# Kernel tuning notes

Hardware: AMD Instinct MI355X
Metric: run time of the kernel (lower is better)

## Reference

```python
import jax, jax.numpy as jnp
import numpy as np


def pixel_coordinates(h, w):
    # (h, w, 2) grid of (x, y) in [-1, 1]
    y = jnp.linspace(-1.0, 1.0, h)
    x = jnp.linspace(-1.0, 1.0, w)
    yy, xx = jnp.meshgrid(y, x, indexing='ij')
    return jnp.stack([xx, yy], axis=-1)


def base_grid(h_in, w_in):
    y = jnp.linspace(-1.0 + 1.0 / h_in, 1.0 - 1.0 / h_in, h_in)
    x = jnp.linspace(-1.0 + 1.0 / w_in, 1.0 - 1.0 / w_in, w_in)
    yy, xx = jnp.meshgrid(y, x, indexing='ij')
    return jnp.stack([xx, yy], axis=-1)  # [h_in, w_in, 2]


def setup_inputs() -> dict:
    key = jax.random.key(0)
    params = jax.random.normal(key, (2, 9, 32, 32), dtype=jnp.float32)
    return {"params": params, "h_out": 128, "w_out": 128}


def reference(params, h_out, w_out):
    B, _, h_in, w_in = params.shape
    N = h_in * w_in
    p = jnp.transpose(params, (0, 2, 3, 1))  # [B, h_in, w_in, 9]

    # positions (mu): base grid + tanh(offset) * (2/h_in)
    mu = base_grid(h_in, w_in)[None] + jnp.tanh(p[..., 0:2]) * (2.0 / h_in)
    mu = mu.reshape(B, N, 2)

    # covariance via Cholesky-like factor L = [[exp(a), 0], [b, exp(c)]]
    v1x = jnp.exp(p[..., 2])
    v2x = p[..., 3]
    v2y = jnp.exp(p[..., 4])
    zero = jnp.zeros_like(v1x)
    L = jnp.stack([jnp.stack([v1x, zero], axis=-1),
                   jnp.stack([v2x, v2y], axis=-1)], axis=-2)  # [B,h,w,2,2]
    cov = L @ jnp.swapaxes(L, -1, -2)
    cov = cov.reshape(B, N, 2, 2) + jnp.eye(2, dtype=params.dtype) * 1e-5
    Sigma_inv = jnp.linalg.inv(cov)  # [B, N, 2, 2]

    colors = jax.nn.sigmoid(p[..., 5:8]).reshape(B, N, 3)
    opacities = jax.nn.sigmoid(p[..., 8]).reshape(B, N)

    coords = pixel_coordinates(h_out, w_out)  # [H, W, 2]
    dx = coords[None, None] - mu[:, :, None, None, :]  # [B, N, H, W, 2]
    exponent = -0.5 * jnp.einsum('bnhwi,bnij,bnhwj->bnhw', dx, Sigma_inv, dx)
    exponent = jnp.clip(exponent, -20.0, 20.0)
    kernel = jnp.exp(exponent)  # [B, N, H, W]

    weights = opacities[:, :, None, None] * kernel
    weights_sum = jnp.sum(weights, axis=1, keepdims=True) + 1e-8
    norm_w = weights / weights_sum  # [B, N, H, W]
    image = jnp.einsum('bnhw,bnc->bchw', norm_w, colors)  # [B, 3, H, W]
    return image
```

## Files before the change

### kernel.cpp

```cpp
#include <hip/hip_runtime.h>


#define NB   2
#define NG   1024
#define HOUT 128
#define WOUT 128
#define PSTRIDE 24
#define NCHUNK 16

typedef float v2f __attribute__((ext_vector_type(2)));

__device__ __forceinline__ float fast_exp(float x) {
    return __builtin_amdgcn_exp2f(x * 1.4426950408889634f);
}
__device__ __forceinline__ float fast_sigmoid(float x) {
    float e = __builtin_amdgcn_exp2f(-x * 1.4426950408889634f);
    return __builtin_amdgcn_rcpf(1.0f + e);
}
__device__ __forceinline__ float fast_tanh(float x) {
    float e = __builtin_amdgcn_exp2f(-x * 2.8853900817779268f);
    return fmaf(2.0f, __builtin_amdgcn_rcpf(1.0f + e), -1.0f);
}

__global__ __launch_bounds__(256) void gauss_setup(const float* __restrict__ params,
                                                   float* __restrict__ gd) {
    int gid = blockIdx.x * blockDim.x + threadIdx.x;
    if (gid >= NB * NG) return;
    int b = gid >> 10;
    int n = gid & (NG - 1);
    int h = n >> 5;
    int w = n & 31;

    const float* P = params + b * 9 * NG + n;
    float p0 = P[0 * NG];
    float p1 = P[1 * NG];
    float p2 = P[2 * NG];
    float p3 = P[3 * NG];
    float p4 = P[4 * NG];
    float p5 = P[5 * NG];
    float p6 = P[6 * NG];
    float p7 = P[7 * NG];
    float p8 = P[8 * NG];

    float mux = -0.96875f + (float)w * 0.0625f + fast_tanh(p0) * 0.0625f;
    float muy = -0.96875f + (float)h * 0.0625f + fast_tanh(p1) * 0.0625f;

    float ea  = fast_exp(p2);
    float ec  = fast_exp(p4);
    float c00 = ea * ea + 1e-5f;
    float c01 = p3 * ea;
    float c11 = p3 * p3 + ec * ec + 1e-5f;
    float det = c00 * c11 - c01 * c01;
    float id  = 1.0f / det;
    float Sa  =  c11 * id;
    float Sb  = -c01 * id;
    float Sc  =  c00 * id;

    const float s = -0.72134752044448169f;
    float A  = s * Sa;
    float B2 = 2.0f * s * Sb;
    float C  = s * Sc;

    float cr = fast_sigmoid(p5);
    float cg = fast_sigmoid(p6);
    float cb = fast_sigmoid(p7);
    float op = fast_sigmoid(p8);

    float* o = gd + ((size_t)b * (NG / 2) + (n >> 1)) * PSTRIDE + (n & 1);
    o[0]  = mux;  o[2]  = muy;  o[4]  = A;       o[6]  = B2;
    o[8]  = C;    o[10] = op;   o[12] = op * cr; o[14] = op * cg;
    o[16] = op * cb;
}

__global__ __launch_bounds__(1024, 8) void gauss_render(const float* __restrict__ gd,
                                                        float* __restrict__ out) {
    __shared__ float4 sred[1024];

    const int tx  = threadIdx.x;
    const int ty  = threadIdx.y;
    const int tid = ty * 64 + tx;
    const int blk = blockIdx.x;
    const int b   = blk >> 8;
    const int pix = ((blk & 255) << 6) + tx;

    const int h = pix >> 7;
    const int w = pix & 127;
    const float px = -1.0f + (float)w * (2.0f / 127.0f);
    const float py = -1.0f + (float)h * (2.0f / 127.0f);
    const v2f px2 = {px, px};
    const v2f py2 = {py, py};

    const int chunk = __builtin_amdgcn_readfirstlane(ty);
    const v2f* __restrict__ gp = (const v2f*)(gd
        + (size_t)b * (NG / 2) * PSTRIDE
        + (size_t)chunk * (NG / 2 / NCHUNK) * PSTRIDE);

    v2f wsum2 = {0.0f, 0.0f}, ar2 = {0.0f, 0.0f};
    v2f ag2   = {0.0f, 0.0f}, ab2 = {0.0f, 0.0f};

    #pragma unroll 4
    for (int j = 0; j < NG / 2 / NCHUNK; ++j) {
        const v2f* __restrict__ r = gp + j * (PSTRIDE / 2);
        v2f mux2 = r[0], muy2 = r[1];
        v2f A2   = r[2], B22  = r[3], C2 = r[4];
        v2f op2  = r[5], ocr2 = r[6], ocg2 = r[7], ocb2 = r[8];

        v2f dx = px2 - mux2;
        v2f dy = py2 - muy2;
        v2f m  = A2 * dx;
        m      = __builtin_elementwise_fma(B22, dy, m);
        v2f t  = C2 * dy;
        v2f e2 = __builtin_elementwise_fma(t, dy, m * dx);
        e2 = __builtin_elementwise_max(e2, (v2f){-28.853900817779268f,
                                                 -28.853900817779268f});
        v2f k2 = {__builtin_amdgcn_exp2f(e2.x), __builtin_amdgcn_exp2f(e2.y)};

        wsum2 = __builtin_elementwise_fma(op2,  k2, wsum2);
        ar2   = __builtin_elementwise_fma(ocr2, k2, ar2);
        ag2   = __builtin_elementwise_fma(ocg2, k2, ag2);
        ab2   = __builtin_elementwise_fma(ocb2, k2, ab2);
    }

    sred[tid] = make_float4(wsum2.x + wsum2.y, ar2.x + ar2.y,
                            ag2.x + ag2.y,     ab2.x + ab2.y);
    __syncthreads();

    if (ty == 0) {
        float4 a = sred[tx];
        #pragma unroll
        for (int k2i = 1; k2i < NCHUNK; ++k2i) {
            float4 t = sred[k2i * 64 + tx];
            a.x += t.x; a.y += t.y; a.z += t.z; a.w += t.w;
        }
        float inv = 1.0f / (a.x + 1e-8f);
        float* ob = out + b * 3 * (HOUT * WOUT) + pix;
        ob[0]               = a.y * inv;
        ob[HOUT * WOUT]     = a.z * inv;
        ob[2 * HOUT * WOUT] = a.w * inv;
    }
}

extern "C" void kernel_launch(void* const* d_in, const int* in_sizes, int n_in,
                              void* d_out, int out_size, void* d_ws, size_t ws_size,
                              hipStream_t stream) {
    const float* params = (const float*)d_in[0];
    float* gd  = (float*)d_ws;
    float* out = (float*)d_out;

    hipLaunchKernelGGL(gauss_setup, dim3((NB * NG + 255) / 256), dim3(256), 0, stream,
                       params, gd);
    hipLaunchKernelGGL(gauss_render, dim3(NB * (HOUT * WOUT) / 64), dim3(64, 16), 0,
                       stream, gd, out);
}
```

Baseline: 70.44 us.

## Fuse gaussian setup into render kernel with per-block LDS parameter table

Removes the separate setup kernel. Each 1024-thread render block now recomputes all 1024 gaussians' parameters for its batch into shared memory and then reads them from LDS instead of global memory. This drops one kernel launch and the global round trip, but every one of the 512 blocks redoes the setup math and pays a block-wide barrier before rendering. The packed stride shrinks from 24 to 20 floats to cut LDS use, and the loop unroll drops from 4 to 2.

```diff
diff --git a/kernel.cpp b/kernel.cpp
--- a/kernel.cpp
+++ b/kernel.cpp
@@ -5,7 +5,7 @@
 #define NG   1024
 #define HOUT 128
 #define WOUT 128
-#define PSTRIDE 24
+#define PSTRIDE 20
 #define NCHUNK 16
 
 typedef float v2f __attribute__((ext_vector_type(2)));
@@ -22,58 +22,9 @@
     return fmaf(2.0f, __builtin_amdgcn_rcpf(1.0f + e), -1.0f);
 }
 
-__global__ __launch_bounds__(256) void gauss_setup(const float* __restrict__ params,
-                                                   float* __restrict__ gd) {
-    int gid = blockIdx.x * blockDim.x + threadIdx.x;
-    if (gid >= NB * NG) return;
-    int b = gid >> 10;
-    int n = gid & (NG - 1);
-    int h = n >> 5;
-    int w = n & 31;
-
-    const float* P = params + b * 9 * NG + n;
-    float p0 = P[0 * NG];
-    float p1 = P[1 * NG];
-    float p2 = P[2 * NG];
-    float p3 = P[3 * NG];
-    float p4 = P[4 * NG];
-    float p5 = P[5 * NG];
-    float p6 = P[6 * NG];
-    float p7 = P[7 * NG];
-    float p8 = P[8 * NG];
-
-    float mux = -0.96875f + (float)w * 0.0625f + fast_tanh(p0) * 0.0625f;
-    float muy = -0.96875f + (float)h * 0.0625f + fast_tanh(p1) * 0.0625f;
-
-    float ea  = fast_exp(p2);
-    float ec  = fast_exp(p4);
-    float c00 = ea * ea + 1e-5f;
-    float c01 = p3 * ea;
-    float c11 = p3 * p3 + ec * ec + 1e-5f;
-    float det = c00 * c11 - c01 * c01;
-    float id  = 1.0f / det;
-    float Sa  =  c11 * id;
-    float Sb  = -c01 * id;
-    float Sc  =  c00 * id;
-
-    const float s = -0.72134752044448169f;
-    float A  = s * Sa;
-    float B2 = 2.0f * s * Sb;
-    float C  = s * Sc;
-
-    float cr = fast_sigmoid(p5);
-    float cg = fast_sigmoid(p6);
-    float cb = fast_sigmoid(p7);
-    float op = fast_sigmoid(p8);
-
-    float* o = gd + ((size_t)b * (NG / 2) + (n >> 1)) * PSTRIDE + (n & 1);
-    o[0]  = mux;  o[2]  = muy;  o[4]  = A;       o[6]  = B2;
-    o[8]  = C;    o[10] = op;   o[12] = op * cr; o[14] = op * cg;
-    o[16] = op * cb;
-}
-
-__global__ __launch_bounds__(1024, 8) void gauss_render(const float* __restrict__ gd,
-                                                        float* __restrict__ out) {
+__global__ __launch_bounds__(1024, 8) void gauss_fused(const float* __restrict__ params,
+                                                       float* __restrict__ out) {
+    __shared__ __align__(16) float gtab[(NG / 2) * PSTRIDE];
     __shared__ float4 sred[1024];
 
     const int tx  = threadIdx.x;
@@ -81,8 +32,55 @@
     const int tid = ty * 64 + tx;
     const int blk = blockIdx.x;
     const int b   = blk >> 8;
+
+    {
+        const int n = tid;
+        const int gh = n >> 5;
+        const int gw = n & 31;
+
+        const float* P = params + b * 9 * NG + n;
+        float p0 = P[0 * NG];
+        float p1 = P[1 * NG];
+        float p2 = P[2 * NG];
+        float p3 = P[3 * NG];
+        float p4 = P[4 * NG];
+        float p5 = P[5 * NG];
+        float p6 = P[6 * NG];
+        float p7 = P[7 * NG];
+        float p8 = P[8 * NG];
+
+        float mux = -0.96875f + (float)gw * 0.0625f + fast_tanh(p0) * 0.0625f;
+        float muy = -0.96875f + (float)gh * 0.0625f + fast_tanh(p1) * 0.0625f;
+
+        float ea  = fast_exp(p2);
+        float ec  = fast_exp(p4);
+        float c00 = ea * ea + 1e-5f;
+        float c01 = p3 * ea;
+        float c11 = p3 * p3 + ec * ec + 1e-5f;
+        float det = c00 * c11 - c01 * c01;
+        float id  = 1.0f / det;
+        float Sa  =  c11 * id;
+        float Sb  = -c01 * id;
+        float Sc  =  c00 * id;
+
+        const float s = -0.72134752044448169f;
+        float A  = s * Sa;
+        float B2 = 2.0f * s * Sb;
+        float C  = s * Sc;
+
+        float cr = fast_sigmoid(p5);
+        float cg = fast_sigmoid(p6);
+        float cb = fast_sigmoid(p7);
+        float op = fast_sigmoid(p8);
+
+        float* o = gtab + (n >> 1) * PSTRIDE + (n & 1);
+        o[0]  = mux;  o[2]  = muy;  o[4]  = A;       o[6]  = B2;
+        o[8]  = C;    o[10] = op;   o[12] = op * cr; o[14] = op * cg;
+        o[16] = op * cb;
+    }
+    __syncthreads();
+
     const int pix = ((blk & 255) << 6) + tx;
-
     const int h = pix >> 7;
     const int w = pix & 127;
     const float px = -1.0f + (float)w * (2.0f / 127.0f);
@@ -90,15 +88,13 @@
     const v2f px2 = {px, px};
     const v2f py2 = {py, py};
 
-    const int chunk = __builtin_amdgcn_readfirstlane(ty);
-    const v2f* __restrict__ gp = (const v2f*)(gd
-        + (size_t)b * (NG / 2) * PSTRIDE
-        + (size_t)chunk * (NG / 2 / NCHUNK) * PSTRIDE);
+    const v2f* __restrict__ gp =
+        (const v2f*)(gtab + ty * (NG / 2 / NCHUNK) * PSTRIDE);
 
     v2f wsum2 = {0.0f, 0.0f}, ar2 = {0.0f, 0.0f};
     v2f ag2   = {0.0f, 0.0f}, ab2 = {0.0f, 0.0f};
 
-    #pragma unroll 4
+    #pragma unroll 2
     for (int j = 0; j < NG / 2 / NCHUNK; ++j) {
         const v2f* __restrict__ r = gp + j * (PSTRIDE / 2);
         v2f mux2 = r[0], muy2 = r[1];
@@ -144,11 +140,9 @@
                               void* d_out, int out_size, void* d_ws, size_t ws_size,
                               hipStream_t stream) {
     const float* params = (const float*)d_in[0];
-    float* gd  = (float*)d_ws;
     float* out = (float*)d_out;
+    (void)d_ws; (void)ws_size;
 
-    hipLaunchKernelGGL(gauss_setup, dim3((NB * NG + 255) / 256), dim3(256), 0, stream,
-                       params, gd);
-    hipLaunchKernelGGL(gauss_render, dim3(NB * (HOUT * WOUT) / 64), dim3(64, 16), 0,
-                       stream, gd, out);
+    hipLaunchKernelGGL(gauss_fused, dim3(NB * (HOUT * WOUT) / 64), dim3(64, 16),
+                       0, stream, params, out);
 }
```

New measurement: 68.01 us. 1.04x faster.
